# Performance work log

Hardware: AMD Instinct MI355X
Metric: run time of the kernel (lower is better)

The kernel has to match this reference:

```python
import jax, jax.numpy as jnp
import numpy as np

FEAT = 36          # 4 + node_embedding_dim(32)
N_NODES = 24       # max_num_nodes_per_route
N_ROUTES = 48      # max_num_route
CUST_H = 128
CUST_OUT = 32
RNN_H = 128        # route_output_dim
B = 512


def _xavier(key, shape):
    fan_in, fan_out = shape[0], shape[1]
    lim = float(np.sqrt(6.0 / (fan_in + fan_out)))
    return jax.random.uniform(key, shape, jnp.float32, -lim, lim)


def setup_inputs() -> dict:
    key = jax.random.key(0)
    ks = jax.random.split(key, 24)
    inp = {
        "candidates": jax.random.normal(ks[0], (B, 2 * FEAT), jnp.float32),
        "customers": jax.random.normal(ks[1], (B, N_ROUTES, N_NODES * FEAT), jnp.float32),
        # Customer_Model MLP: 36 -> 128 (tanh) -> 32 (tanh)
        "cust_w1": _xavier(ks[2], (FEAT, CUST_H)),
        "cust_b1": jnp.zeros((CUST_H,), jnp.float32),
        "cust_w2": _xavier(ks[3], (CUST_H, CUST_OUT)),
        "cust_b2": jnp.zeros((CUST_OUT,), jnp.float32),
        # GRU layer 0 (input 32 -> hidden 128), gates order (r,z,n)
        "gru_wih0": _xavier(ks[4], (CUST_OUT, 3 * RNN_H)),
        "gru_whh0": _xavier(ks[5], (RNN_H, 3 * RNN_H)),
        "gru_bih0": jnp.zeros((3 * RNN_H,), jnp.float32),
        "gru_bhh0": jnp.zeros((3 * RNN_H,), jnp.float32),
        # GRU layer 1 (128 -> 128)
        "gru_wih1": _xavier(ks[6], (RNN_H, 3 * RNN_H)),
        "gru_whh1": _xavier(ks[7], (RNN_H, 3 * RNN_H)),
        "gru_bih1": jnp.zeros((3 * RNN_H,), jnp.float32),
        "gru_bhh1": jnp.zeros((3 * RNN_H,), jnp.float32),
        # candidate head and final MLP
        "cand_w": _xavier(ks[8], (2 * FEAT, 64)),
        "cand_b": jnp.zeros((64,), jnp.float32),
        "fc1_w": _xavier(ks[9], (RNN_H + 64, 128)),
        "fc1_b": jnp.zeros((128,), jnp.float32),
        "fc2_w": _xavier(ks[10], (128, 128)),
        "fc2_b": jnp.zeros((128,), jnp.float32),
        "fc3_w": _xavier(ks[11], (128, 1)),
        "fc3_b": jnp.zeros((1,), jnp.float32),
    }
    return inp


def _gru_layer(x_seq, wih, whh, bih, bhh):
    # x_seq: [T, N, in_dim]; returns [T, N, RNN_H]
    gi = jnp.einsum('tni,ih->tnh', x_seq, wih) + bih  # precompute input gates

    def step(h, gi_t):
        gh = h @ whh + bhh
        i_r, i_z, i_n = jnp.split(gi_t, 3, axis=-1)
        h_r, h_z, h_n = jnp.split(gh, 3, axis=-1)
        r = jax.nn.sigmoid(i_r + h_r)
        z = jax.nn.sigmoid(i_z + h_z)
        n = jnp.tanh(i_n + r * h_n)
        h_new = (1.0 - z) * n + z * h
        return h_new, h_new

    h0 = jnp.zeros((x_seq.shape[1], RNN_H), x_seq.dtype)
    _, out = jax.lax.scan(step, h0, gi)
    return out


def reference(candidates, customers, cust_w1, cust_b1, cust_w2, cust_b2,
              gru_wih0, gru_whh0, gru_bih0, gru_bhh0,
              gru_wih1, gru_whh1, gru_bih1, gru_bhh1,
              cand_w, cand_b, fc1_w, fc1_b, fc2_w, fc2_b, fc3_w, fc3_b):
    b = candidates.shape[0]
    x_c = candidates @ cand_w + cand_b                      # [B, 64]

    # all routes processed at once: fold routes into batch dim
    x = customers.reshape(b * N_ROUTES, N_NODES, FEAT)
    x = jnp.transpose(x, (1, 0, 2))                          # [T=24, B*48, 36]
    # Customer_Model MLP (tanh hidden, tanh output)
    x = jnp.tanh(jnp.tanh(x @ cust_w1 + cust_b1) @ cust_w2 + cust_b2)  # [24, B*48, 32]

    out = _gru_layer(x, gru_wih0, gru_whh0, gru_bih0, gru_bhh0)
    out = _gru_layer(out, gru_wih1, gru_whh1, gru_bih1, gru_bhh1)
    last = out[-1].reshape(b, N_ROUTES, RNN_H)               # last timestep per route
    x_r = last.mean(axis=1)                                  # mean over 48 routes
    # dropout is identity at inference

    h = jnp.concatenate([x_r, x_c], axis=1)                  # [B, 192]
    h = jnp.tanh(h @ fc1_w + fc1_b)
    h = jnp.tanh(h @ fc2_w + fc2_b)
    return h @ fc3_w + fc3_b                                 # [B, 1]
```

## Files before the change

kernel.cpp:

```cpp
#include <hip/hip_runtime.h>
#include <stdint.h>


#define NSEQ   24576
#define TSTEPS 24

typedef __attribute__((ext_vector_type(8))) short bf16x8;
typedef __attribute__((ext_vector_type(4))) float floatx4;

#define PK_W1    0
#define PK_W2    8192
#define PK_WIH0  12288
#define PK_WHH0  24576
#define PK_WIH1  73728
#define PK_WHH1  122880
#define PK_END   172032
#define X2_EL    172032
#define HOUT_BYTE 38092800

#define MFMA(a,b,c) c = __builtin_amdgcn_mfma_f32_16x16x32_bf16(a, b, c, 0, 0, 0)

__device__ __forceinline__ uint16_t f2bf(float f) {
  uint32_t u = __float_as_uint(f);
  u += 0x7FFFu + ((u >> 16) & 1u);
  return (uint16_t)(u >> 16);
}
__device__ __forceinline__ float fast_sigmoid(float x) {
  float e = __builtin_amdgcn_exp2f(-1.4426950408889634f * x);
  return __builtin_amdgcn_rcpf(1.0f + e);
}
__device__ __forceinline__ float fast_tanh(float x) {
  float e = __builtin_amdgcn_exp2f(-2.8853900817779268f * x);
  return 2.0f * __builtin_amdgcn_rcpf(1.0f + e) - 1.0f;
}
__device__ __forceinline__ bf16x8 ldf(const uint16_t* p) {
  return *(const bf16x8*)p;
}

__global__ __launch_bounds__(256) void pack_weights(
    const float* __restrict__ w1, const float* __restrict__ w2,
    const float* __restrict__ wih0, const float* __restrict__ whh0,
    const float* __restrict__ wih1, const float* __restrict__ whh1,
    uint16_t* __restrict__ ws) {
  int idx = blockIdx.x * 256 + threadIdx.x;
  if (idx >= PK_END) return;
  const float* W; int N, KB, Kreal, base;
  if      (idx <  8192) { W = w1;   N = 128; KB = 2; Kreal = 36;  base = 0; }
  else if (idx < 12288) { W = w2;   N = 32;  KB = 4; Kreal = 128; base = 8192; }
  else if (idx < 24576) { W = wih0; N = 384; KB = 1; Kreal = 32;  base = 12288; }
  else if (idx < 73728) { W = whh0; N = 384; KB = 4; Kreal = 128; base = 24576; }
  else if (idx < 122880){ W = wih1; N = 384; KB = 4; Kreal = 128; base = 73728; }
  else                  { W = whh1; N = 384; KB = 4; Kreal = 128; base = 122880; }
  int li = idx - base;
  int frag = li >> 9;
  int e = li & 511;
  int lane = e >> 3, j = e & 7;
  int kb = frag % KB, nt = frag / KB;
  int k = kb * 32 + (lane >> 4) * 8 + j;
  int n = nt * 16 + (lane & 15);
  float v = (k < Kreal) ? W[k * N + n] : 0.0f;
  ws[base + li] = f2bf(v);
}

__global__ __launch_bounds__(256) void mlp_kernel(
    const float* __restrict__ customers, const float* __restrict__ b1,
    const float* __restrict__ b2, const uint16_t* __restrict__ wpk,
    uint16_t* __restrict__ x2out) {
  __shared__ uint16_t sA[128 * 136];
  const int r0 = blockIdx.x * 128;
  const int t  = r0 / NSEQ;
  const int s0 = r0 % NSEQ;
  const int tid = threadIdx.x;
  const int w = tid >> 6, l = tid & 63, q = l >> 4, c = l & 15;
  const int lo8 = l * 8;

  float b1r[8], b2r[2];
  #pragma unroll
  for (int nt = 0; nt < 8; ++nt) b1r[nt] = b1[nt * 16 + c];
  b2r[0] = b2[c]; b2r[1] = b2[16 + c];

  floatx4 acc[2][8];
  #pragma unroll
  for (int mi = 0; mi < 2; ++mi)
    #pragma unroll
    for (int nt = 0; nt < 8; ++nt) acc[mi][nt] = (floatx4){0.f, 0.f, 0.f, 0.f};

  #pragma unroll
  for (int mi = 0; mi < 2; ++mi) {
    const int mt = 2 * w + mi;
    const int seq = s0 + mt * 16 + c;
    const float* xp = customers + (size_t)seq * 864 + t * 36;
    floatx4 u0 = *(const floatx4*)(xp + q * 8);
    floatx4 u1 = *(const floatx4*)(xp + q * 8 + 4);
    bf16x8 a0;
    a0[0] = (short)f2bf(u0[0]); a0[1] = (short)f2bf(u0[1]);
    a0[2] = (short)f2bf(u0[2]); a0[3] = (short)f2bf(u0[3]);
    a0[4] = (short)f2bf(u1[0]); a0[5] = (short)f2bf(u1[1]);
    a0[6] = (short)f2bf(u1[2]); a0[7] = (short)f2bf(u1[3]);
    bf16x8 a1x = (bf16x8){0,0,0,0,0,0,0,0};
    if (q == 0) {
      floatx4 u2 = *(const floatx4*)(xp + 32);
      a1x[0] = (short)f2bf(u2[0]); a1x[1] = (short)f2bf(u2[1]);
      a1x[2] = (short)f2bf(u2[2]); a1x[3] = (short)f2bf(u2[3]);
    }
    #pragma unroll
    for (int nt = 0; nt < 8; ++nt) {
      bf16x8 bv0 = ldf(wpk + PK_W1 + (nt * 2 + 0) * 512 + lo8);
      bf16x8 bv1 = ldf(wpk + PK_W1 + (nt * 2 + 1) * 512 + lo8);
      MFMA(a0,  bv0, acc[mi][nt]);
      MFMA(a1x, bv1, acc[mi][nt]);
    }
  }
  #pragma unroll
  for (int mi = 0; mi < 2; ++mi) {
    const int mt = 2 * w + mi;
    #pragma unroll
    for (int nt = 0; nt < 8; ++nt)
      #pragma unroll
      for (int e = 0; e < 4; ++e) {
        float v = fast_tanh(acc[mi][nt][e] + b1r[nt]);
        sA[(mt * 16 + q * 4 + e) * 136 + nt * 16 + c] = f2bf(v);
      }
  }
  __syncthreads();

  floatx4 acc2[2][2];
  #pragma unroll
  for (int mi = 0; mi < 2; ++mi)
    #pragma unroll
    for (int nt = 0; nt < 2; ++nt) acc2[mi][nt] = (floatx4){0.f, 0.f, 0.f, 0.f};

  #pragma unroll
  for (int kb = 0; kb < 4; ++kb) {
    bf16x8 av0 = ldf(&sA[((2 * w + 0) * 16 + c) * 136 + kb * 32 + q * 8]);
    bf16x8 av1 = ldf(&sA[((2 * w + 1) * 16 + c) * 136 + kb * 32 + q * 8]);
    #pragma unroll
    for (int nt = 0; nt < 2; ++nt) {
      bf16x8 bv = ldf(wpk + PK_W2 + (nt * 4 + kb) * 512 + lo8);
      MFMA(av0, bv, acc2[0][nt]);
      MFMA(av1, bv, acc2[1][nt]);
    }
  }
  #pragma unroll
  for (int mi = 0; mi < 2; ++mi) {
    const int mt = 2 * w + mi;
    #pragma unroll
    for (int nt = 0; nt < 2; ++nt)
      #pragma unroll
      for (int e = 0; e < 4; ++e) {
        float v = fast_tanh(acc2[mi][nt][e] + b2r[nt]);
        int m = mt * 16 + q * 4 + e;
        x2out[(size_t)(r0 + m) * 32 + nt * 16 + c] = f2bf(v);
      }
  }
}

__global__ __launch_bounds__(512, 2) void gru_res(
    const uint16_t* __restrict__ wpk, const uint16_t* __restrict__ x2,
    const float* __restrict__ bih0, const float* __restrict__ bhh0,
    const float* __restrict__ bih1, const float* __restrict__ bhh1,
    float* __restrict__ hout) {
  __shared__ uint16_t hl[2][2][32 * 136];
  const int seq0 = blockIdx.x * 32;
  const int tid = threadIdx.x;
  const int J = tid >> 6, l = tid & 63, q = l >> 4, c = l & 15;
  const int lo8 = l * 8;

  { uint32_t* z = (uint32_t*)hl;
    for (int i = tid; i < 8704; i += 512) z[i] = 0u; }

  bf16x8 wi0[3], wh0[3][4], wi1[3][4], wh1[3][4];
  #pragma unroll
  for (int g = 0; g < 3; ++g) {
    wi0[g] = ldf(wpk + PK_WIH0 + (g * 8 + J) * 512 + lo8);
    #pragma unroll
    for (int kb = 0; kb < 4; ++kb) {
      wh0[g][kb] = ldf(wpk + PK_WHH0 + ((g * 8 + J) * 4 + kb) * 512 + lo8);
      wi1[g][kb] = ldf(wpk + PK_WIH1 + ((g * 8 + J) * 4 + kb) * 512 + lo8);
      wh1[g][kb] = ldf(wpk + PK_WHH1 + ((g * 8 + J) * 4 + kb) * 512 + lo8);
    }
  }
  const int col = J * 16 + c;
  const float bR0 = bih0[col]       + bhh0[col];
  const float bZ0 = bih0[128 + col] + bhh0[128 + col];
  const float bN0 = bih0[256 + col];
  const float bH0 = bhh0[256 + col];
  const float bR1 = bih1[col]       + bhh1[col];
  const float bZ1 = bih1[128 + col] + bhh1[128 + col];
  const float bN1 = bih1[256 + col];
  const float bH1 = bhh1[256 + col];

  floatx4 h0m[2], h1m[2];
  h0m[0] = (floatx4){0.f, 0.f, 0.f, 0.f}; h0m[1] = (floatx4){0.f, 0.f, 0.f, 0.f};
  h1m[0] = (floatx4){0.f, 0.f, 0.f, 0.f}; h1m[1] = (floatx4){0.f, 0.f, 0.f, 0.f};

  bf16x8 axc[2];
  axc[0] = ldf(x2 + (size_t)(seq0 + c) * 32 + q * 8);
  axc[1] = ldf(x2 + (size_t)(seq0 + 16 + c) * 32 + q * 8);
  __syncthreads();

  #pragma unroll 1
  for (int t = 0; t < TSTEPS; ++t) {
    const int cur = t & 1, prv = cur ^ 1;
    const int tn = (t < TSTEPS - 1) ? t + 1 : t;
    bf16x8 axn0 = ldf(x2 + ((size_t)tn * NSEQ + seq0 + c) * 32 + q * 8);
    bf16x8 axn1 = ldf(x2 + ((size_t)tn * NSEQ + seq0 + 16 + c) * 32 + q * 8);

    uint16_t* h0w = hl[0][cur]; const uint16_t* h0r = hl[0][prv];
    uint16_t* h1w = hl[1][cur]; const uint16_t* h1r = hl[1][prv];

    {
      floatx4 aR[2], aZ[2], aN[2], aH[2];
      #pragma unroll
      for (int mi = 0; mi < 2; ++mi) {
        aR[mi] = (floatx4){bR0, bR0, bR0, bR0};
        aZ[mi] = (floatx4){bZ0, bZ0, bZ0, bZ0};
        aN[mi] = (floatx4){bN0, bN0, bN0, bN0};
        aH[mi] = (floatx4){bH0, bH0, bH0, bH0};
      }
      #pragma unroll
      for (int kb = 0; kb < 4; ++kb) {
        bf16x8 a0 = ldf(h0r + (c)      * 136 + kb * 32 + q * 8);
        bf16x8 a1 = ldf(h0r + (16 + c) * 136 + kb * 32 + q * 8);
        MFMA(a0, wh0[0][kb], aR[0]); MFMA(a1, wh0[0][kb], aR[1]);
        MFMA(a0, wh0[1][kb], aZ[0]); MFMA(a1, wh0[1][kb], aZ[1]);
        MFMA(a0, wh0[2][kb], aH[0]); MFMA(a1, wh0[2][kb], aH[1]);
      }
      MFMA(axc[0], wi0[0], aR[0]); MFMA(axc[1], wi0[0], aR[1]);
      MFMA(axc[0], wi0[1], aZ[0]); MFMA(axc[1], wi0[1], aZ[1]);
      MFMA(axc[0], wi0[2], aN[0]); MFMA(axc[1], wi0[2], aN[1]);
      #pragma unroll
      for (int mi = 0; mi < 2; ++mi)
        #pragma unroll
        for (int e = 0; e < 4; ++e) {
          float r  = fast_sigmoid(aR[mi][e]);
          float zz = fast_sigmoid(aZ[mi][e]);
          float nn = fast_tanh(aN[mi][e] + r * aH[mi][e]);
          float hv = nn + zz * (h0m[mi][e] - nn);
          h0m[mi][e] = hv;
          h0w[(mi * 16 + q * 4 + e) * 136 + J * 16 + c] = f2bf(hv);
        }
    }
    __syncthreads();

    {
      floatx4 aR[2], aZ[2], aN[2], aH[2];
      #pragma unroll
      for (int mi = 0; mi < 2; ++mi) {
        aR[mi] = (floatx4){bR1, bR1, bR1, bR1};
        aZ[mi] = (floatx4){bZ1, bZ1, bZ1, bZ1};
        aN[mi] = (floatx4){bN1, bN1, bN1, bN1};
        aH[mi] = (floatx4){bH1, bH1, bH1, bH1};
      }
      #pragma unroll
      for (int kb = 0; kb < 4; ++kb) {
        bf16x8 ai0 = ldf(h0w + (c)      * 136 + kb * 32 + q * 8);
        bf16x8 ai1 = ldf(h0w + (16 + c) * 136 + kb * 32 + q * 8);
        bf16x8 ah0 = ldf(h1r + (c)      * 136 + kb * 32 + q * 8);
        bf16x8 ah1 = ldf(h1r + (16 + c) * 136 + kb * 32 + q * 8);
        MFMA(ai0, wi1[0][kb], aR[0]); MFMA(ai1, wi1[0][kb], aR[1]);
        MFMA(ai0, wi1[1][kb], aZ[0]); MFMA(ai1, wi1[1][kb], aZ[1]);
        MFMA(ai0, wi1[2][kb], aN[0]); MFMA(ai1, wi1[2][kb], aN[1]);
        MFMA(ah0, wh1[0][kb], aR[0]); MFMA(ah1, wh1[0][kb], aR[1]);
        MFMA(ah0, wh1[1][kb], aZ[0]); MFMA(ah1, wh1[1][kb], aZ[1]);
        MFMA(ah0, wh1[2][kb], aH[0]); MFMA(ah1, wh1[2][kb], aH[1]);
      }
      #pragma unroll
      for (int mi = 0; mi < 2; ++mi)
        #pragma unroll
        for (int e = 0; e < 4; ++e) {
          float r  = fast_sigmoid(aR[mi][e]);
          float zz = fast_sigmoid(aZ[mi][e]);
          float nn = fast_tanh(aN[mi][e] + r * aH[mi][e]);
          float hv = nn + zz * (h1m[mi][e] - nn);
          h1m[mi][e] = hv;
          h1w[(mi * 16 + q * 4 + e) * 136 + J * 16 + c] = f2bf(hv);
        }
    }
    __syncthreads();
    axc[0] = axn0; axc[1] = axn1;
  }

  #pragma unroll
  for (int mi = 0; mi < 2; ++mi)
    #pragma unroll
    for (int e = 0; e < 4; ++e) {
      int seq = seq0 + mi * 16 + q * 4 + e;
      hout[(size_t)seq * 128 + J * 16 + c] = h1m[mi][e];
    }
}

__global__ __launch_bounds__(192) void final_kernel(
    const float* __restrict__ hout, const float* __restrict__ cands,
    const float* __restrict__ cw, const float* __restrict__ cb,
    const float* __restrict__ f1w, const float* __restrict__ f1b,
    const float* __restrict__ f2w, const float* __restrict__ f2b,
    const float* __restrict__ f3w, const float* __restrict__ f3b,
    float* __restrict__ out) {
  __shared__ float hc[192];
  __shared__ float v1[128];
  __shared__ float v2[128];
  __shared__ float red[128];
  const int b = blockIdx.x, tid = threadIdx.x;
  if (tid < 128) {
    float s = 0.f;
    const float* hp = hout + (size_t)(b * 48) * 128 + tid;
    #pragma unroll 4
    for (int r = 0; r < 48; ++r) s += hp[r * 128];
    hc[tid] = s * (1.0f / 48.0f);
  } else {
    int j = tid - 128;
    float s = cb[j];
    const float* cp = cands + b * 72;
    #pragma unroll 8
    for (int k = 0; k < 72; ++k) s += cp[k] * cw[k * 64 + j];
    hc[128 + j] = s;
  }
  __syncthreads();
  if (tid < 128) {
    float s = f1b[tid];
    for (int k = 0; k < 192; ++k) s += hc[k] * f1w[k * 128 + tid];
    v1[tid] = fast_tanh(s);
  }
  __syncthreads();
  if (tid < 128) {
    float s = f2b[tid];
    for (int k = 0; k < 128; ++k) s += v1[k] * f2w[k * 128 + tid];
    v2[tid] = fast_tanh(s);
  }
  __syncthreads();
  if (tid < 128) red[tid] = v2[tid] * f3w[tid];
  __syncthreads();
  if (tid < 64) {
    float s = red[tid] + red[tid + 64];
    s += __shfl_down(s, 32);
    s += __shfl_down(s, 16);
    s += __shfl_down(s, 8);
    s += __shfl_down(s, 4);
    s += __shfl_down(s, 2);
    s += __shfl_down(s, 1);
    if (tid == 0) out[b] = s + f3b[0];
  }
}

extern "C" void kernel_launch(void* const* d_in, const int* in_sizes, int n_in,
                              void* d_out, int out_size, void* d_ws, size_t ws_size,
                              hipStream_t stream) {
  const float* cand  = (const float*)d_in[0];
  const float* cust  = (const float*)d_in[1];
  const float* w1    = (const float*)d_in[2];
  const float* b1    = (const float*)d_in[3];
  const float* w2    = (const float*)d_in[4];
  const float* b2    = (const float*)d_in[5];
  const float* wih0  = (const float*)d_in[6];
  const float* whh0  = (const float*)d_in[7];
  const float* bih0  = (const float*)d_in[8];
  const float* bhh0  = (const float*)d_in[9];
  const float* wih1  = (const float*)d_in[10];
  const float* whh1  = (const float*)d_in[11];
  const float* bih1  = (const float*)d_in[12];
  const float* bhh1  = (const float*)d_in[13];
  const float* cw    = (const float*)d_in[14];
  const float* cb    = (const float*)d_in[15];
  const float* f1w   = (const float*)d_in[16];
  const float* f1b   = (const float*)d_in[17];
  const float* f2w   = (const float*)d_in[18];
  const float* f2b   = (const float*)d_in[19];
  const float* f3w   = (const float*)d_in[20];
  const float* f3b   = (const float*)d_in[21];

  uint16_t* wsp = (uint16_t*)d_ws;
  uint16_t* x2p = wsp + X2_EL;
  float* hout = (float*)((char*)d_ws + HOUT_BYTE);
  float* outp = (float*)d_out;

  pack_weights<<<(PK_END + 255) / 256, 256, 0, stream>>>(w1, w2, wih0, whh0, wih1, whh1, wsp);
  mlp_kernel<<<(NSEQ * TSTEPS) / 128, 256, 0, stream>>>(cust, b1, b2, wsp, x2p);
  gru_res<<<NSEQ / 32, 512, 0, stream>>>(wsp, x2p, bih0, bhh0, bih1, bhh1, hout);
  final_kernel<<<512, 192, 0, stream>>>(hout, cand, cw, cb, f1w, f1b, f2w, f2b, f3w, f3b, outp);
}
```

Measured before the change: 428.9 us.

## Pipeline the two GRU layers across separate wave groups in one block

The fused two-layer GRU kernel is restructured so that waves 0–7 run layer 0 and waves 8–15 run layer 1, each one timestep apart, in a 1024-thread block. Each step now needs only one block barrier instead of two, and the two layers' MFMA and gate work can overlap. Layer 1's input weights are no longer held in registers but reloaded from global memory on every step, which eases register pressure at higher occupancy. The cost is repeated cache traffic for those weights and an extra pipeline step.

```diff
diff --git a/kernel.cpp b/kernel.cpp
--- a/kernel.cpp
+++ b/kernel.cpp
@@ -155,139 +155,152 @@
   }
 }
 
-__global__ __launch_bounds__(512, 2) void gru_res(
+__global__ __launch_bounds__(1024, 4) void gru_lp(
     const uint16_t* __restrict__ wpk, const uint16_t* __restrict__ x2,
     const float* __restrict__ bih0, const float* __restrict__ bhh0,
     const float* __restrict__ bih1, const float* __restrict__ bhh1,
     float* __restrict__ hout) {
-  __shared__ uint16_t hl[2][2][32 * 136];
+  __shared__ uint16_t hl0[2][32 * 136];
+  __shared__ uint16_t hl1[2][32 * 136];
   const int seq0 = blockIdx.x * 32;
   const int tid = threadIdx.x;
-  const int J = tid >> 6, l = tid & 63, q = l >> 4, c = l & 15;
+  const int wv = tid >> 6, l = tid & 63, q = l >> 4, c = l & 15;
+  const int layer = wv >> 3, J = wv & 7;
   const int lo8 = l * 8;
 
-  { uint32_t* z = (uint32_t*)hl;
-    for (int i = tid; i < 8704; i += 512) z[i] = 0u; }
-
-  bf16x8 wi0[3], wh0[3][4], wi1[3][4], wh1[3][4];
-  #pragma unroll
-  for (int g = 0; g < 3; ++g) {
-    wi0[g] = ldf(wpk + PK_WIH0 + (g * 8 + J) * 512 + lo8);
-    #pragma unroll
-    for (int kb = 0; kb < 4; ++kb) {
-      wh0[g][kb] = ldf(wpk + PK_WHH0 + ((g * 8 + J) * 4 + kb) * 512 + lo8);
-      wi1[g][kb] = ldf(wpk + PK_WIH1 + ((g * 8 + J) * 4 + kb) * 512 + lo8);
-      wh1[g][kb] = ldf(wpk + PK_WHH1 + ((g * 8 + J) * 4 + kb) * 512 + lo8);
-    }
-  }
+  { uint32_t* z0 = (uint32_t*)hl0;
+    for (int i = tid; i < 2 * 32 * 68; i += 1024) z0[i] = 0u;
+    uint32_t* z1 = (uint32_t*)hl1;
+    for (int i = tid; i < 2 * 32 * 68; i += 1024) z1[i] = 0u; }
+
+  floatx4 hm[2];
+  hm[0] = (floatx4){0.f, 0.f, 0.f, 0.f};
+  hm[1] = (floatx4){0.f, 0.f, 0.f, 0.f};
+
   const int col = J * 16 + c;
-  const float bR0 = bih0[col]       + bhh0[col];
-  const float bZ0 = bih0[128 + col] + bhh0[128 + col];
-  const float bN0 = bih0[256 + col];
-  const float bH0 = bhh0[256 + col];
-  const float bR1 = bih1[col]       + bhh1[col];
-  const float bZ1 = bih1[128 + col] + bhh1[128 + col];
-  const float bN1 = bih1[256 + col];
-  const float bH1 = bhh1[256 + col];
-
-  floatx4 h0m[2], h1m[2];
-  h0m[0] = (floatx4){0.f, 0.f, 0.f, 0.f}; h0m[1] = (floatx4){0.f, 0.f, 0.f, 0.f};
-  h1m[0] = (floatx4){0.f, 0.f, 0.f, 0.f}; h1m[1] = (floatx4){0.f, 0.f, 0.f, 0.f};
-
-  bf16x8 axc[2];
-  axc[0] = ldf(x2 + (size_t)(seq0 + c) * 32 + q * 8);
-  axc[1] = ldf(x2 + (size_t)(seq0 + 16 + c) * 32 + q * 8);
+  float bR, bZ, bN, bH;
+  bf16x8 wi0[3], wh0[3][4];
+  bf16x8 wh1[3][4];
+  bf16x8 axc0, axc1;
+
+  if (layer == 0) {
+    #pragma unroll
+    for (int g = 0; g < 3; ++g) {
+      wi0[g] = ldf(wpk + PK_WIH0 + (g * 8 + J) * 512 + lo8);
+      #pragma unroll
+      for (int kb = 0; kb < 4; ++kb)
+        wh0[g][kb] = ldf(wpk + PK_WHH0 + ((g * 8 + J) * 4 + kb) * 512 + lo8);
+    }
+    bR = bih0[col]       + bhh0[col];
+    bZ = bih0[128 + col] + bhh0[128 + col];
+    bN = bih0[256 + col];
+    bH = bhh0[256 + col];
+    axc0 = ldf(x2 + (size_t)(seq0 + c) * 32 + q * 8);
+    axc1 = ldf(x2 + (size_t)(seq0 + 16 + c) * 32 + q * 8);
+  } else {
+    #pragma unroll
+    for (int g = 0; g < 3; ++g)
+      #pragma unroll
+      for (int kb = 0; kb < 4; ++kb)
+        wh1[g][kb] = ldf(wpk + PK_WHH1 + ((g * 8 + J) * 4 + kb) * 512 + lo8);
+    bR = bih1[col]       + bhh1[col];
+    bZ = bih1[128 + col] + bhh1[128 + col];
+    bN = bih1[256 + col];
+    bH = bhh1[256 + col];
+  }
   __syncthreads();
 
   #pragma unroll 1
-  for (int t = 0; t < TSTEPS; ++t) {
-    const int cur = t & 1, prv = cur ^ 1;
-    const int tn = (t < TSTEPS - 1) ? t + 1 : t;
-    bf16x8 axn0 = ldf(x2 + ((size_t)tn * NSEQ + seq0 + c) * 32 + q * 8);
-    bf16x8 axn1 = ldf(x2 + ((size_t)tn * NSEQ + seq0 + 16 + c) * 32 + q * 8);
-
-    uint16_t* h0w = hl[0][cur]; const uint16_t* h0r = hl[0][prv];
-    uint16_t* h1w = hl[1][cur]; const uint16_t* h1r = hl[1][prv];
-
-    {
-      floatx4 aR[2], aZ[2], aN[2], aH[2];
-      #pragma unroll
-      for (int mi = 0; mi < 2; ++mi) {
-        aR[mi] = (floatx4){bR0, bR0, bR0, bR0};
-        aZ[mi] = (floatx4){bZ0, bZ0, bZ0, bZ0};
-        aN[mi] = (floatx4){bN0, bN0, bN0, bN0};
-        aH[mi] = (floatx4){bH0, bH0, bH0, bH0};
-      }
-      #pragma unroll
-      for (int kb = 0; kb < 4; ++kb) {
-        bf16x8 a0 = ldf(h0r + (c)      * 136 + kb * 32 + q * 8);
-        bf16x8 a1 = ldf(h0r + (16 + c) * 136 + kb * 32 + q * 8);
-        MFMA(a0, wh0[0][kb], aR[0]); MFMA(a1, wh0[0][kb], aR[1]);
-        MFMA(a0, wh0[1][kb], aZ[0]); MFMA(a1, wh0[1][kb], aZ[1]);
-        MFMA(a0, wh0[2][kb], aH[0]); MFMA(a1, wh0[2][kb], aH[1]);
-      }
-      MFMA(axc[0], wi0[0], aR[0]); MFMA(axc[1], wi0[0], aR[1]);
-      MFMA(axc[0], wi0[1], aZ[0]); MFMA(axc[1], wi0[1], aZ[1]);
-      MFMA(axc[0], wi0[2], aN[0]); MFMA(axc[1], wi0[2], aN[1]);
-      #pragma unroll
-      for (int mi = 0; mi < 2; ++mi)
-        #pragma unroll
-        for (int e = 0; e < 4; ++e) {
-          float r  = fast_sigmoid(aR[mi][e]);
-          float zz = fast_sigmoid(aZ[mi][e]);
-          float nn = fast_tanh(aN[mi][e] + r * aH[mi][e]);
-          float hv = nn + zz * (h0m[mi][e] - nn);
-          h0m[mi][e] = hv;
-          h0w[(mi * 16 + q * 4 + e) * 136 + J * 16 + c] = f2bf(hv);
+  for (int p = 0; p <= TSTEPS; ++p) {
+    const int cw = p & 1, pv = cw ^ 1;
+    if (layer == 0) {
+      if (p < TSTEPS) {
+        const int tn = (p < TSTEPS - 1) ? p + 1 : p;
+        bf16x8 axn0 = ldf(x2 + ((size_t)tn * NSEQ + seq0 + c) * 32 + q * 8);
+        bf16x8 axn1 = ldf(x2 + ((size_t)tn * NSEQ + seq0 + 16 + c) * 32 + q * 8);
+        floatx4 aR[2], aZ[2], aN[2], aH[2];
+        #pragma unroll
+        for (int mi = 0; mi < 2; ++mi) {
+          aR[mi] = (floatx4){bR, bR, bR, bR};
+          aZ[mi] = (floatx4){bZ, bZ, bZ, bZ};
+          aN[mi] = (floatx4){bN, bN, bN, bN};
+          aH[mi] = (floatx4){bH, bH, bH, bH};
         }
+        #pragma unroll
+        for (int kb = 0; kb < 4; ++kb) {
+          bf16x8 a0 = ldf(&hl0[pv][(c)      * 136 + kb * 32 + q * 8]);
+          bf16x8 a1 = ldf(&hl0[pv][(16 + c) * 136 + kb * 32 + q * 8]);
+          MFMA(a0, wh0[0][kb], aR[0]); MFMA(a1, wh0[0][kb], aR[1]);
+          MFMA(a0, wh0[1][kb], aZ[0]); MFMA(a1, wh0[1][kb], aZ[1]);
+          MFMA(a0, wh0[2][kb], aH[0]); MFMA(a1, wh0[2][kb], aH[1]);
+        }
+        MFMA(axc0, wi0[0], aR[0]); MFMA(axc1, wi0[0], aR[1]);
+        MFMA(axc0, wi0[1], aZ[0]); MFMA(axc1, wi0[1], aZ[1]);
+        MFMA(axc0, wi0[2], aN[0]); MFMA(axc1, wi0[2], aN[1]);
+        #pragma unroll
+        for (int mi = 0; mi < 2; ++mi)
+          #pragma unroll
+          for (int e = 0; e < 4; ++e) {
+            float r  = fast_sigmoid(aR[mi][e]);
+            float zz = fast_sigmoid(aZ[mi][e]);
+            float nn = fast_tanh(aN[mi][e] + r * aH[mi][e]);
+            float hv = nn + zz * (hm[mi][e] - nn);
+            hm[mi][e] = hv;
+            hl0[cw][(mi * 16 + q * 4 + e) * 136 + J * 16 + c] = f2bf(hv);
+          }
+        axc0 = axn0; axc1 = axn1;
+      }
+    } else {
+      if (p > 0) {
+        floatx4 aR[2], aZ[2], aN[2], aH[2];
+        #pragma unroll
+        for (int mi = 0; mi < 2; ++mi) {
+          aR[mi] = (floatx4){bR, bR, bR, bR};
+          aZ[mi] = (floatx4){bZ, bZ, bZ, bZ};
+          aN[mi] = (floatx4){bN, bN, bN, bN};
+          aH[mi] = (floatx4){bH, bH, bH, bH};
+        }
+        #pragma unroll
+        for (int kb = 0; kb < 4; ++kb) {
+          bf16x8 ai0 = ldf(&hl0[pv][(c)      * 136 + kb * 32 + q * 8]);
+          bf16x8 ai1 = ldf(&hl0[pv][(16 + c) * 136 + kb * 32 + q * 8]);
+          bf16x8 ah0 = ldf(&hl1[cw][(c)      * 136 + kb * 32 + q * 8]);
+          bf16x8 ah1 = ldf(&hl1[cw][(16 + c) * 136 + kb * 32 + q * 8]);
+          bf16x8 w_r = ldf(wpk + PK_WIH1 + ((0 * 8 + J) * 4 + kb) * 512 + lo8);
+          bf16x8 w_z = ldf(wpk + PK_WIH1 + ((1 * 8 + J) * 4 + kb) * 512 + lo8);
+          bf16x8 w_n = ldf(wpk + PK_WIH1 + ((2 * 8 + J) * 4 + kb) * 512 + lo8);
+          MFMA(ai0, w_r, aR[0]); MFMA(ai1, w_r, aR[1]);
+          MFMA(ai0, w_z, aZ[0]); MFMA(ai1, w_z, aZ[1]);
+          MFMA(ai0, w_n, aN[0]); MFMA(ai1, w_n, aN[1]);
+          MFMA(ah0, wh1[0][kb], aR[0]); MFMA(ah1, wh1[0][kb], aR[1]);
+          MFMA(ah0, wh1[1][kb], aZ[0]); MFMA(ah1, wh1[1][kb], aZ[1]);
+          MFMA(ah0, wh1[2][kb], aH[0]); MFMA(ah1, wh1[2][kb], aH[1]);
+        }
+        #pragma unroll
+        for (int mi = 0; mi < 2; ++mi)
+          #pragma unroll
+          for (int e = 0; e < 4; ++e) {
+            float r  = fast_sigmoid(aR[mi][e]);
+            float zz = fast_sigmoid(aZ[mi][e]);
+            float nn = fast_tanh(aN[mi][e] + r * aH[mi][e]);
+            float hv = nn + zz * (hm[mi][e] - nn);
+            hm[mi][e] = hv;
+            hl1[pv][(mi * 16 + q * 4 + e) * 136 + J * 16 + c] = f2bf(hv);
+          }
+      }
     }
     __syncthreads();
-
-    {
-      floatx4 aR[2], aZ[2], aN[2], aH[2];
-      #pragma unroll
-      for (int mi = 0; mi < 2; ++mi) {
-        aR[mi] = (floatx4){bR1, bR1, bR1, bR1};
-        aZ[mi] = (floatx4){bZ1, bZ1, bZ1, bZ1};
-        aN[mi] = (floatx4){bN1, bN1, bN1, bN1};
-        aH[mi] = (floatx4){bH1, bH1, bH1, bH1};
-      }
-      #pragma unroll
-      for (int kb = 0; kb < 4; ++kb) {
-        bf16x8 ai0 = ldf(h0w + (c)      * 136 + kb * 32 + q * 8);
-        bf16x8 ai1 = ldf(h0w + (16 + c) * 136 + kb * 32 + q * 8);
-        bf16x8 ah0 = ldf(h1r + (c)      * 136 + kb * 32 + q * 8);
-        bf16x8 ah1 = ldf(h1r + (16 + c) * 136 + kb * 32 + q * 8);
-        MFMA(ai0, wi1[0][kb], aR[0]); MFMA(ai1, wi1[0][kb], aR[1]);
-        MFMA(ai0, wi1[1][kb], aZ[0]); MFMA(ai1, wi1[1][kb], aZ[1]);
-        MFMA(ai0, wi1[2][kb], aN[0]); MFMA(ai1, wi1[2][kb], aN[1]);
-        MFMA(ah0, wh1[0][kb], aR[0]); MFMA(ah1, wh1[0][kb], aR[1]);
-        MFMA(ah0, wh1[1][kb], aZ[0]); MFMA(ah1, wh1[1][kb], aZ[1]);
-        MFMA(ah0, wh1[2][kb], aH[0]); MFMA(ah1, wh1[2][kb], aH[1]);
-      }
-      #pragma unroll
-      for (int mi = 0; mi < 2; ++mi)
-        #pragma unroll
-        for (int e = 0; e < 4; ++e) {
-          float r  = fast_sigmoid(aR[mi][e]);
-          float zz = fast_sigmoid(aZ[mi][e]);
-          float nn = fast_tanh(aN[mi][e] + r * aH[mi][e]);
-          float hv = nn + zz * (h1m[mi][e] - nn);
-          h1m[mi][e] = hv;
-          h1w[(mi * 16 + q * 4 + e) * 136 + J * 16 + c] = f2bf(hv);
-        }
-    }
-    __syncthreads();
-    axc[0] = axn0; axc[1] = axn1;
-  }
-
-  #pragma unroll
-  for (int mi = 0; mi < 2; ++mi)
-    #pragma unroll
-    for (int e = 0; e < 4; ++e) {
-      int seq = seq0 + mi * 16 + q * 4 + e;
-      hout[(size_t)seq * 128 + J * 16 + c] = h1m[mi][e];
-    }
+  }
+
+  if (layer == 1) {
+    #pragma unroll
+    for (int mi = 0; mi < 2; ++mi)
+      #pragma unroll
+      for (int e = 0; e < 4; ++e) {
+        int seq = seq0 + mi * 16 + q * 4 + e;
+        hout[(size_t)seq * 128 + J * 16 + c] = hm[mi][e];
+      }
+  }
 }
 
 __global__ __launch_bounds__(192) void final_kernel(
@@ -376,6 +389,6 @@
 
   pack_weights<<<(PK_END + 255) / 256, 256, 0, stream>>>(w1, w2, wih0, whh0, wih1, whh1, wsp);
   mlp_kernel<<<(NSEQ * TSTEPS) / 128, 256, 0, stream>>>(cust, b1, b2, wsp, x2p);
-  gru_res<<<NSEQ / 32, 512, 0, stream>>>(wsp, x2p, bih0, bhh0, bih1, bhh1, hout);
+  gru_lp<<<NSEQ / 32, 1024, 0, stream>>>(wsp, x2p, bih0, bhh0, bih1, bhh1, hout);
   final_kernel<<<512, 192, 0, stream>>>(hout, cand, cw, cb, f1w, f1b, f2w, f2b, f3w, f3b, outp);
 }
```

After: 1.230 ms. +186.8%, slower.

## Skew GRU layers in time to halve barriers per step

Applied to the files above, without the earlier changes.

Layer 0 is peeled for the first step and then runs one timestep ahead of layer 1. Each loop iteration now computes layer 1 at step t and layer 0 at step t+1 with a single barrier, both reading shared-memory state from the previous phase. This removes one __syncthreads per timestep and lets the two independent layer computations interleave for more MFMA overlap. In exchange it adds a prologue and needs separate double-buffered hidden-state arrays per layer.

```diff
diff --git a/kernel.cpp b/kernel.cpp
--- a/kernel.cpp
+++ b/kernel.cpp
@@ -155,19 +155,22 @@
   }
 }
 
-__global__ __launch_bounds__(512, 2) void gru_res(
+__global__ __launch_bounds__(512, 2) void gru_mg(
     const uint16_t* __restrict__ wpk, const uint16_t* __restrict__ x2,
     const float* __restrict__ bih0, const float* __restrict__ bhh0,
     const float* __restrict__ bih1, const float* __restrict__ bhh1,
     float* __restrict__ hout) {
-  __shared__ uint16_t hl[2][2][32 * 136];
+  __shared__ uint16_t hl0[2][32 * 136];
+  __shared__ uint16_t hl1[2][32 * 136];
   const int seq0 = blockIdx.x * 32;
   const int tid = threadIdx.x;
   const int J = tid >> 6, l = tid & 63, q = l >> 4, c = l & 15;
   const int lo8 = l * 8;
 
-  { uint32_t* z = (uint32_t*)hl;
-    for (int i = tid; i < 8704; i += 512) z[i] = 0u; }
+  { uint32_t* z0 = (uint32_t*)hl0;
+    for (int i = tid; i < 2 * 32 * 68; i += 512) z0[i] = 0u;
+    uint32_t* z1 = (uint32_t*)hl1;
+    for (int i = tid; i < 2 * 32 * 68; i += 512) z1[i] = 0u; }
 
   bf16x8 wi0[3], wh0[3][4], wi1[3][4], wh1[3][4];
   #pragma unroll
@@ -194,22 +197,82 @@
   h0m[0] = (floatx4){0.f, 0.f, 0.f, 0.f}; h0m[1] = (floatx4){0.f, 0.f, 0.f, 0.f};
   h1m[0] = (floatx4){0.f, 0.f, 0.f, 0.f}; h1m[1] = (floatx4){0.f, 0.f, 0.f, 0.f};
 
-  bf16x8 axc[2];
-  axc[0] = ldf(x2 + (size_t)(seq0 + c) * 32 + q * 8);
-  axc[1] = ldf(x2 + (size_t)(seq0 + 16 + c) * 32 + q * 8);
+  __syncthreads();
+
+  {
+    bf16x8 ax0 = ldf(x2 + (size_t)(seq0 + c) * 32 + q * 8);
+    bf16x8 ax1 = ldf(x2 + (size_t)(seq0 + 16 + c) * 32 + q * 8);
+    floatx4 aR[2], aZ[2], aN[2];
+    #pragma unroll
+    for (int mi = 0; mi < 2; ++mi) {
+      aR[mi] = (floatx4){bR0, bR0, bR0, bR0};
+      aZ[mi] = (floatx4){bZ0, bZ0, bZ0, bZ0};
+      aN[mi] = (floatx4){bN0, bN0, bN0, bN0};
+    }
+    MFMA(ax0, wi0[0], aR[0]); MFMA(ax1, wi0[0], aR[1]);
+    MFMA(ax0, wi0[1], aZ[0]); MFMA(ax1, wi0[1], aZ[1]);
+    MFMA(ax0, wi0[2], aN[0]); MFMA(ax1, wi0[2], aN[1]);
+    #pragma unroll
+    for (int mi = 0; mi < 2; ++mi)
+      #pragma unroll
+      for (int e = 0; e < 4; ++e) {
+        float r  = fast_sigmoid(aR[mi][e]);
+        float zz = fast_sigmoid(aZ[mi][e]);
+        float nn = fast_tanh(aN[mi][e] + r * bH0);
+        float hv = nn - zz * nn;
+        h0m[mi][e] = hv;
+        hl0[0][(mi * 16 + q * 4 + e) * 136 + J * 16 + c] = f2bf(hv);
+      }
+  }
   __syncthreads();
 
   #pragma unroll 1
   for (int t = 0; t < TSTEPS; ++t) {
-    const int cur = t & 1, prv = cur ^ 1;
-    const int tn = (t < TSTEPS - 1) ? t + 1 : t;
-    bf16x8 axn0 = ldf(x2 + ((size_t)tn * NSEQ + seq0 + c) * 32 + q * 8);
-    bf16x8 axn1 = ldf(x2 + ((size_t)tn * NSEQ + seq0 + 16 + c) * 32 + q * 8);
-
-    uint16_t* h0w = hl[0][cur]; const uint16_t* h0r = hl[0][prv];
-    uint16_t* h1w = hl[1][cur]; const uint16_t* h1r = hl[1][prv];
+    const int cur = t & 1, nxt = cur ^ 1;
+    const uint16_t* hA = hl0[cur];
+    const uint16_t* hB = hl1[nxt];
+    uint16_t* w1p = hl1[cur];
+    uint16_t* w0p = hl0[nxt];
+    const int tx = (t < TSTEPS - 1) ? t + 1 : t;
+    bf16x8 ax0 = ldf(x2 + ((size_t)tx * NSEQ + seq0 + c) * 32 + q * 8);
+    bf16x8 ax1 = ldf(x2 + ((size_t)tx * NSEQ + seq0 + 16 + c) * 32 + q * 8);
 
     {
+      floatx4 aR[2], aZ[2], aN[2], aH[2];
+      #pragma unroll
+      for (int mi = 0; mi < 2; ++mi) {
+        aR[mi] = (floatx4){bR1, bR1, bR1, bR1};
+        aZ[mi] = (floatx4){bZ1, bZ1, bZ1, bZ1};
+        aN[mi] = (floatx4){bN1, bN1, bN1, bN1};
+        aH[mi] = (floatx4){bH1, bH1, bH1, bH1};
+      }
+      #pragma unroll
+      for (int kb = 0; kb < 4; ++kb) {
+        bf16x8 a0 = ldf(hA + (c)      * 136 + kb * 32 + q * 8);
+        bf16x8 a1 = ldf(hA + (16 + c) * 136 + kb * 32 + q * 8);
+        bf16x8 b0 = ldf(hB + (c)      * 136 + kb * 32 + q * 8);
+        bf16x8 b1 = ldf(hB + (16 + c) * 136 + kb * 32 + q * 8);
+        MFMA(a0, wi1[0][kb], aR[0]); MFMA(a1, wi1[0][kb], aR[1]);
+        MFMA(a0, wi1[1][kb], aZ[0]); MFMA(a1, wi1[1][kb], aZ[1]);
+        MFMA(a0, wi1[2][kb], aN[0]); MFMA(a1, wi1[2][kb], aN[1]);
+        MFMA(b0, wh1[0][kb], aR[0]); MFMA(b1, wh1[0][kb], aR[1]);
+        MFMA(b0, wh1[1][kb], aZ[0]); MFMA(b1, wh1[1][kb], aZ[1]);
+        MFMA(b0, wh1[2][kb], aH[0]); MFMA(b1, wh1[2][kb], aH[1]);
+      }
+      #pragma unroll
+      for (int mi = 0; mi < 2; ++mi)
+        #pragma unroll
+        for (int e = 0; e < 4; ++e) {
+          float r  = fast_sigmoid(aR[mi][e]);
+          float zz = fast_sigmoid(aZ[mi][e]);
+          float nn = fast_tanh(aN[mi][e] + r * aH[mi][e]);
+          float hv = nn + zz * (h1m[mi][e] - nn);
+          h1m[mi][e] = hv;
+          w1p[(mi * 16 + q * 4 + e) * 136 + J * 16 + c] = f2bf(hv);
+        }
+    }
+
+    if (t < TSTEPS - 1) {
       floatx4 aR[2], aZ[2], aN[2], aH[2];
       #pragma unroll
       for (int mi = 0; mi < 2; ++mi) {
@@ -220,15 +283,15 @@
       }
       #pragma unroll
       for (int kb = 0; kb < 4; ++kb) {
-        bf16x8 a0 = ldf(h0r + (c)      * 136 + kb * 32 + q * 8);
-        bf16x8 a1 = ldf(h0r + (16 + c) * 136 + kb * 32 + q * 8);
+        bf16x8 a0 = ldf(hA + (c)      * 136 + kb * 32 + q * 8);
+        bf16x8 a1 = ldf(hA + (16 + c) * 136 + kb * 32 + q * 8);
         MFMA(a0, wh0[0][kb], aR[0]); MFMA(a1, wh0[0][kb], aR[1]);
         MFMA(a0, wh0[1][kb], aZ[0]); MFMA(a1, wh0[1][kb], aZ[1]);
         MFMA(a0, wh0[2][kb], aH[0]); MFMA(a1, wh0[2][kb], aH[1]);
       }
-      MFMA(axc[0], wi0[0], aR[0]); MFMA(axc[1], wi0[0], aR[1]);
-      MFMA(axc[0], wi0[1], aZ[0]); MFMA(axc[1], wi0[1], aZ[1]);
-      MFMA(axc[0], wi0[2], aN[0]); MFMA(axc[1], wi0[2], aN[1]);
+      MFMA(ax0, wi0[0], aR[0]); MFMA(ax1, wi0[0], aR[1]);
+      MFMA(ax0, wi0[1], aZ[0]); MFMA(ax1, wi0[1], aZ[1]);
+      MFMA(ax0, wi0[2], aN[0]); MFMA(ax1, wi0[2], aN[1]);
       #pragma unroll
       for (int mi = 0; mi < 2; ++mi)
         #pragma unroll
@@ -238,47 +301,10 @@
           float nn = fast_tanh(aN[mi][e] + r * aH[mi][e]);
           float hv = nn + zz * (h0m[mi][e] - nn);
           h0m[mi][e] = hv;
-          h0w[(mi * 16 + q * 4 + e) * 136 + J * 16 + c] = f2bf(hv);
+          w0p[(mi * 16 + q * 4 + e) * 136 + J * 16 + c] = f2bf(hv);
         }
     }
     __syncthreads();
-
-    {
-      floatx4 aR[2], aZ[2], aN[2], aH[2];
-      #pragma unroll
-      for (int mi = 0; mi < 2; ++mi) {
-        aR[mi] = (floatx4){bR1, bR1, bR1, bR1};
-        aZ[mi] = (floatx4){bZ1, bZ1, bZ1, bZ1};
-        aN[mi] = (floatx4){bN1, bN1, bN1, bN1};
-        aH[mi] = (floatx4){bH1, bH1, bH1, bH1};
-      }
-      #pragma unroll
-      for (int kb = 0; kb < 4; ++kb) {
-        bf16x8 ai0 = ldf(h0w + (c)      * 136 + kb * 32 + q * 8);
-        bf16x8 ai1 = ldf(h0w + (16 + c) * 136 + kb * 32 + q * 8);
-        bf16x8 ah0 = ldf(h1r + (c)      * 136 + kb * 32 + q * 8);
-        bf16x8 ah1 = ldf(h1r + (16 + c) * 136 + kb * 32 + q * 8);
-        MFMA(ai0, wi1[0][kb], aR[0]); MFMA(ai1, wi1[0][kb], aR[1]);
-        MFMA(ai0, wi1[1][kb], aZ[0]); MFMA(ai1, wi1[1][kb], aZ[1]);
-        MFMA(ai0, wi1[2][kb], aN[0]); MFMA(ai1, wi1[2][kb], aN[1]);
-        MFMA(ah0, wh1[0][kb], aR[0]); MFMA(ah1, wh1[0][kb], aR[1]);
-        MFMA(ah0, wh1[1][kb], aZ[0]); MFMA(ah1, wh1[1][kb], aZ[1]);
-        MFMA(ah0, wh1[2][kb], aH[0]); MFMA(ah1, wh1[2][kb], aH[1]);
-      }
-      #pragma unroll
-      for (int mi = 0; mi < 2; ++mi)
-        #pragma unroll
-        for (int e = 0; e < 4; ++e) {
-          float r  = fast_sigmoid(aR[mi][e]);
-          float zz = fast_sigmoid(aZ[mi][e]);
-          float nn = fast_tanh(aN[mi][e] + r * aH[mi][e]);
-          float hv = nn + zz * (h1m[mi][e] - nn);
-          h1m[mi][e] = hv;
-          h1w[(mi * 16 + q * 4 + e) * 136 + J * 16 + c] = f2bf(hv);
-        }
-    }
-    __syncthreads();
-    axc[0] = axn0; axc[1] = axn1;
   }
 
   #pragma unroll
@@ -376,6 +402,6 @@
 
   pack_weights<<<(PK_END + 255) / 256, 256, 0, stream>>>(w1, w2, wih0, whh0, wih1, whh1, wsp);
   mlp_kernel<<<(NSEQ * TSTEPS) / 128, 256, 0, stream>>>(cust, b1, b2, wsp, x2p);
-  gru_res<<<NSEQ / 32, 512, 0, stream>>>(wsp, x2p, bih0, bhh0, bih1, bhh1, hout);
+  gru_mg<<<NSEQ / 32, 512, 0, stream>>>(wsp, x2p, bih0, bhh0, bih1, bhh1, hout);
   final_kernel<<<512, 192, 0, stream>>>(hout, cand, cw, cb, f1w, f1b, f2w, f2b, f3w, f3b, outp);
 }
```

Result: slower. 465.8 us (+8.6%).
